# Optimization experiments

Measured on AMD Instinct MI355X. Metric: run time of the kernel, lower is better.

The kernel has to match this reference:

```python
import jax, jax.numpy as jnp
import numpy as np

B, T, D = 2, 2048, 2048
H, KV, HD = 16, 4, 128          # n_heads, n_kv_heads, head_dim
THETA = 10000.0
NREP = H // KV


def _rope_tables(t, hd, dtype):
    inv_freq = 1.0 / (THETA ** (jnp.arange(0, hd, 2, dtype=jnp.float32) / hd))
    pos = jnp.arange(t, dtype=jnp.float32)
    freqs = jnp.outer(pos, inv_freq)            # [T, hd/2]
    emb = jnp.concatenate([freqs, freqs], -1)   # [T, hd]
    return jnp.cos(emb).astype(dtype), jnp.sin(emb).astype(dtype)


def _rotate_half(x):
    a, b = x[..., : x.shape[-1] // 2], x[..., x.shape[-1] // 2 :]
    return jnp.concatenate([-b, a], axis=-1)


def setup_inputs() -> dict:
    key = jax.random.key(0)
    kx, kq, kk, kv, ko = jax.random.split(key, 5)
    s = 1.0 / np.sqrt(D)
    return {
        "x": jax.random.normal(kx, (B, T, D), jnp.float32),
        "Wq": jax.random.normal(kq, (D, H * HD), jnp.float32) * s,
        "Wk": jax.random.normal(kk, (D, KV * HD), jnp.float32) * s,
        "Wv": jax.random.normal(kv, (D, KV * HD), jnp.float32) * s,
        "Wo": jax.random.normal(ko, (H * HD, D), jnp.float32) * s,
    }


def reference(x, Wq, Wk, Wv, Wo):
    b, t, _ = x.shape
    # QKV projections (bias=False)
    q = (x @ Wq).reshape(b, t, H, HD).transpose(0, 2, 1, 3)    # [B,H,T,hd]
    k = (x @ Wk).reshape(b, t, KV, HD).transpose(0, 2, 1, 3)   # [B,KV,T,hd]
    v = (x @ Wv).reshape(b, t, KV, HD).transpose(0, 2, 1, 3)   # [B,KV,T,hd]

    cos, sin = _rope_tables(t, HD, x.dtype)                    # [T,hd]
    q = q * cos + _rotate_half(q) * sin
    k = k * cos + _rotate_half(k) * sin

    # GQA: group query heads onto shared KV heads (no KV replication)
    qg = q.reshape(b, KV, NREP, t, HD)                         # [B,KV,R,T,hd]
    scale = HD ** -0.5
    scores = jnp.einsum("bgrth,bgsh->bgrts", qg, k) * scale    # [B,KV,R,T,T]
    causal = jnp.tril(jnp.ones((t, t), bool))
    scores = jnp.where(causal, scores, jnp.finfo(scores.dtype).min)
    attn = jax.nn.softmax(scores.astype(jnp.float32), axis=-1).astype(x.dtype)
    out = jnp.einsum("bgrts,bgsh->bgrth", attn, v)             # [B,KV,R,T,hd]
    out = out.reshape(b, H, t, HD).transpose(0, 2, 1, 3).reshape(b, t, H * HD)
    return out @ Wo
```

## Files before the change

kernel.cpp:

```cpp
#include <hip/hip_runtime.h>
#include <hip/hip_bf16.h>
#include <type_traits>

#define B_ 2
#define T_ 2048
#define DM_ 2048
#define H_ 16
#define KV_ 4
#define HD_ 128
#define M_ 4096
#define QKVN 3072

typedef __attribute__((ext_vector_type(8))) short bf16x8;
typedef __attribute__((ext_vector_type(4))) float f32x4;
typedef __attribute__((ext_vector_type(4))) short s16x4;
typedef unsigned short u16;
typedef unsigned int u32;
typedef __attribute__((address_space(1))) unsigned int as1_u32;
typedef __attribute__((address_space(3))) unsigned int as3_u32;

__device__ inline u16 f2b(float f){
  __hip_bfloat16 h = __float2bfloat16(f);
  return *reinterpret_cast<u16*>(&h);
}
__device__ inline float b2f(u16 u){
  __hip_bfloat16 h = *reinterpret_cast<__hip_bfloat16*>(&u);
  return __bfloat162float(h);
}
__device__ inline f32x4 mfma16(bf16x8 a, bf16x8 b, f32x4 c){
  return __builtin_amdgcn_mfma_f32_16x16x32_bf16(a, b, c, 0, 0, 0);
}

__global__ void cvt_f32_bf16(const float* __restrict__ in, u16* __restrict__ out){
  int i = (blockIdx.x*256 + threadIdx.x)*4;
  float4 v = *reinterpret_cast<const float4*>(in + i);
  s16x4 o;
  o[0] = (short)f2b(v.x); o[1] = (short)f2b(v.y);
  o[2] = (short)f2b(v.z); o[3] = (short)f2b(v.w);
  *reinterpret_cast<s16x4*>(out + i) = o;
}

__global__ void transpose_cvt(const float* __restrict__ W, u16* __restrict__ Wt, int K, int N){
  __shared__ float tile[32][33];
  const int n0 = blockIdx.x*32, k0 = blockIdx.y*32;
  const int tx = threadIdx.x, ty = threadIdx.y;
#pragma unroll
  for (int i=0;i<4;i++)
    tile[ty+8*i][tx] = W[(size_t)(k0+ty+8*i)*N + n0 + tx];
  __syncthreads();
#pragma unroll
  for (int i=0;i<4;i++)
    Wt[(size_t)(n0+ty+8*i)*K + k0 + tx] = f2b(tile[tx][ty+8*i]);
}

__global__ void transpose_v(const u16* __restrict__ vb, u16* __restrict__ vt){
  __shared__ u16 tile[32][33];
  const int t0 = blockIdx.x*32, d0 = blockIdx.y*32, bk = blockIdx.z;
  const int bb = bk >> 2, kv = bk & 3;
  const int tx = threadIdx.x, ty = threadIdx.y;
#pragma unroll
  for (int i=0;i<4;i++)
    tile[ty+8*i][tx] = vb[(size_t)(bb*T_ + t0+ty+8*i)*QKVN + kv*HD_ + d0 + tx];
  __syncthreads();
#pragma unroll
  for (int i=0;i<4;i++)
    vt[(size_t)(bk*HD_ + d0+ty+8*i)*T_ + t0 + tx] = tile[tx][ty+8*i];
}

__global__ void rope_table(float2* __restrict__ tab){
  int idx = blockIdx.x*256 + threadIdx.x;
  int t = idx >> 6, d = idx & 63;
  float inv = exp2f((float)d * -0.2076205059304601f);
  float sn, cs;
  sincosf((float)t * inv, &sn, &cs);
  tab[idx] = float2{cs, sn};
}

__global__ void rope_apply(u16* __restrict__ qk, const float2* __restrict__ tab,
                           int lognh, int stride){
  int idx = blockIdx.x*256 + threadIdx.x;
  int dp = idx & 31;
  int rh = idx >> 5;
  int nh = 1 << lognh;
  int h = rh & (nh-1);
  int row = rh >> lognh;
  if (row >= M_) return;
  int t = row & (T_-1);
  float4 cn = *reinterpret_cast<const float4*>(tab + t*64 + 2*dp);
  size_t base = (size_t)row*stride + h*HD_ + 2*dp;
  u32 lo = *reinterpret_cast<const u32*>(qk + base);
  u32 hi = *reinterpret_cast<const u32*>(qk + base + 64);
  float a0 = b2f(lo & 0xffff), a1 = b2f(lo >> 16);
  float b0 = b2f(hi & 0xffff), b1 = b2f(hi >> 16);
  u32 nlo = (u32)f2b(a0*cn.x - b0*cn.y) | ((u32)f2b(a1*cn.z - b1*cn.w) << 16);
  u32 nhi = (u32)f2b(b0*cn.x + a0*cn.y) | ((u32)f2b(b1*cn.z + a1*cn.w) << 16);
  *reinterpret_cast<u32*>(qk + base)      = nlo;
  *reinterpret_cast<u32*>(qk + base + 64) = nhi;
}

__device__ inline void cstore(float* p, float v){ *p = v; }
__device__ inline void cstore(u16* p, float v){ *p = f2b(v); }

template<typename CT>
__global__ __launch_bounds__(256) void gemm_bt(const u16* __restrict__ A, const u16* __restrict__ BT,
                                               CT* __restrict__ C, int M, int N, int K)
{
  __shared__ u16 Als[128*64];
  __shared__ u16 Bls[128*64];
  const int tid = threadIdx.x;
  const int wave = tid>>6, lane = tid&63;
  const int gl = lane>>4, qcl = lane&15;
  const int gx = gridDim.x;
  int wid = blockIdx.y*gx + blockIdx.x;
  const int cpx = (gx*gridDim.y) >> 3;
  wid = (wid & 7)*cpx + (wid >> 3);
  const int m0 = (wid / gx)*128, n0 = (wid % gx)*128;
  const int wr = (wave>>1)*64, wc = (wave&1)*64;

  f32x4 acc[4][4];
#pragma unroll
  for (int i=0;i<4;i++)
#pragma unroll
    for (int j=0;j<4;j++) acc[i][j] = f32x4{0.f,0.f,0.f,0.f};

  int rowD[4], colD[4];
#pragma unroll
  for (int p=0;p<4;p++){
    const int D = p*4096 + tid*16;
    rowD[p] = D>>7;
    colD[p] = ((((D>>4)&7) ^ (rowD[p]&7)))*8;
  }

  for (int k0=0; k0<K; k0+=64){
    __syncthreads();
#pragma unroll
    for (int p=0;p<4;p++){
      __builtin_amdgcn_global_load_lds((as1_u32*)(A  + (size_t)(m0+rowD[p])*K + k0 + colD[p]),
                                       (as3_u32*)((char*)Als + p*4096 + wave*1024), 16, 0, 0);
      __builtin_amdgcn_global_load_lds((as1_u32*)(BT + (size_t)(n0+rowD[p])*K + k0 + colD[p]),
                                       (as3_u32*)((char*)Bls + p*4096 + wave*1024), 16, 0, 0);
    }
    __syncthreads();

    bf16x8 af[4][2], bfr[4][2];
#pragma unroll
    for (int mi=0;mi<4;mi++)
#pragma unroll
      for (int kk=0;kk<2;kk++){
        const int row = wr + mi*16 + qcl;
        af[mi][kk] = *reinterpret_cast<const bf16x8*>((char*)Als + row*128 + (((kk<<2)+gl) ^ (qcl&7))*16);
      }
#pragma unroll
    for (int ni=0;ni<4;ni++)
#pragma unroll
      for (int kk=0;kk<2;kk++){
        const int row = wc + ni*16 + qcl;
        bfr[ni][kk] = *reinterpret_cast<const bf16x8*>((char*)Bls + row*128 + (((kk<<2)+gl) ^ (qcl&7))*16);
      }
#pragma unroll
    for (int mi=0;mi<4;mi++)
#pragma unroll
      for (int ni=0;ni<4;ni++)
#pragma unroll
        for (int kk=0;kk<2;kk++)
          acc[mi][ni] = mfma16(af[mi][kk], bfr[ni][kk], acc[mi][ni]);
  }

#pragma unroll
  for (int mi=0;mi<4;mi++)
#pragma unroll
    for (int ni=0;ni<4;ni++)
#pragma unroll
      for (int j=0;j<4;j++){
        int row = m0 + wr + mi*16 + (lane>>4)*4 + j;
        int col = n0 + wc + ni*16 + (lane&15);
        cstore(C + (size_t)row*N + col, acc[mi][ni][j]);
      }
}

__device__ inline const u16* slot_cptr(const u16* pout, const u16* pwt, int u){
  return (u < 4096) ? (pout + (size_t)u*4096) : (pwt + (size_t)(u-4096)*4096);
}

__global__ __launch_bounds__(256, 3) void attn_kernel(const u16* __restrict__ qkv,
                                                      const u16* __restrict__ Vt,
                                                      u16* __restrict__ pout,
                                                      u16* __restrict__ pwt,
                                                      float* __restrict__ ml,
                                                      u16* __restrict__ ao)
{
  __shared__ u16 Ktile[2][4096];
  __shared__ u16 Vtile[2][4096];
  __shared__ u16 plds[4][32*40];
  const int wave = threadIdx.x>>6, lane = threadIdx.x&63;
  const int g = lane>>4, qc = lane&15;

  const int bh = blockIdx.x & 31;
  const int rem = blockIdx.x >> 5;
  int q4, e;
  if (rem < 4)       { q4=0; e=rem; }
  else if (rem < 12) { q4=1; e=rem-4; }
  else if (rem < 24) { q4=2; e=rem-12; }
  else               { q4=3; e=rem-24; }
  const int j  = q4*4 + e/(q4+1);
  const int c  = e%(q4+1);
  const int nc = q4 + 1;
  const int qt = j*4 + wave;
  const int ntg = j*4 + 4;
  const int tstart = 16*c;
  const int tcnt = min(16, ntg - tstart);

  const int h = bh & (H_-1), b = bh >> 4;
  const int kv = h >> 2;

  const u16* qbase = qkv + (size_t)(b*T_ + qt*32)*QKVN + h*HD_ + 8*g;
  bf16x8 qf[2][4];
#pragma unroll
  for (int qs=0; qs<2; qs++)
#pragma unroll
    for (int d4=0; d4<4; d4++)
      qf[qs][d4] = *reinterpret_cast<const bf16x8*>(qbase + (size_t)(qs*16+qc)*QKVN + d4*32);

  const char* Kbase = (const char*)(qkv + (size_t)(b*T_)*QKVN + 2048 + kv*HD_);
  const char* Vbase = (const char*)(Vt + (size_t)(b*KV_+kv)*HD_*T_);
  const char* Ktc = (const char*)&Ktile[0][0];
  const char* Vtc = (const char*)&Vtile[0][0];

  f32x4 oacc[2][8];
#pragma unroll
  for (int qs=0; qs<2; qs++)
#pragma unroll
    for (int dt=0; dt<8; dt++) oacc[qs][dt] = f32x4{0.f,0.f,0.f,0.f};
  float mrun[2] = {-1e30f, -1e30f};
  float lrun[2] = {0.f, 0.f};
  const float SCALE = 0.08838834764831845f;
  const float L2E = 1.4426950408889634f;
  const float DEFER = 8.f;
  u16* pw = &plds[wave][0];

  auto compute = [&](int t, int half, auto mc){
    constexpr bool masked = decltype(mc)::value;
    const int s0 = t*32;
    const int hb = half*8192;
    f32x4 sacc[2][2];
#pragma unroll
    for (int qs=0; qs<2; qs++)
#pragma unroll
      for (int ss=0; ss<2; ss++) sacc[qs][ss] = f32x4{0.f,0.f,0.f,0.f};
    __builtin_amdgcn_s_setprio(1);
#pragma unroll
    for (int d4=0; d4<4; d4++)
#pragma unroll
      for (int ss=0; ss<2; ss++){
        int A = ((ss*16+qc)<<8) + (d4<<6) + (g<<4);
        A ^= (qc&7)<<4;
        bf16x8 kf = *reinterpret_cast<const bf16x8*>(Ktc + hb + A);
#pragma unroll
        for (int qs=0; qs<2; qs++)
          sacc[qs][ss] = mfma16(kf, qf[qs][d4], sacc[qs][ss]);
      }
    __builtin_amdgcn_s_setprio(0);

    float p[2][8], al[2], mnew[2];
#pragma unroll
    for (int qs=0; qs<2; qs++){
      float tm = -1e30f;
#pragma unroll
      for (int ss=0; ss<2; ss++)
#pragma unroll
        for (int jj=0; jj<4; jj++){
          float v = sacc[qs][ss][jj]*SCALE;
          if constexpr (masked){
            int sg = s0 + ss*16 + g*4 + jj;
            if (sg > qt*32 + qs*16 + qc) v = -1e30f;
          }
          p[qs][ss*4+jj] = v;
          tm = fmaxf(tm, v);
        }
      tm = fmaxf(tm, __shfl_xor(tm, 16));
      tm = fmaxf(tm, __shfl_xor(tm, 32));
      mnew[qs] = fmaxf(mrun[qs], tm);
      if (tm - mrun[qs] <= DEFER) mnew[qs] = mrun[qs];
      al[qs] = exp2f((mrun[qs]-mnew[qs])*L2E);
    }
#pragma unroll
    for (int qs=0; qs<2; qs++){
      float rs = 0.f;
#pragma unroll
      for (int i=0;i<8;i++){ p[qs][i] = exp2f((p[qs][i]-mnew[qs])*L2E); rs += p[qs][i]; }
      rs += __shfl_xor(rs, 16);
      rs += __shfl_xor(rs, 32);
      lrun[qs] = lrun[qs]*al[qs] + rs;
      mrun[qs] = mnew[qs];
    }
    if (!__all((al[0]==1.f) & (al[1]==1.f))){
      float aj0[4], aj1[4];
#pragma unroll
      for (int jj=0; jj<4; jj++){
        aj0[jj] = __shfl(al[0], g*4+jj);
        aj1[jj] = __shfl(al[1], g*4+jj);
      }
#pragma unroll
      for (int dt=0; dt<8; dt++)
#pragma unroll
        for (int jj=0; jj<4; jj++){
          oacc[0][dt][jj] *= aj0[jj];
          oacc[1][dt][jj] *= aj1[jj];
        }
    }
#pragma unroll
    for (int qs=0; qs<2; qs++)
#pragma unroll
      for (int ss=0; ss<2; ss++){
        unsigned w0 = (unsigned)f2b(p[qs][ss*4+0]) | ((unsigned)f2b(p[qs][ss*4+1])<<16);
        unsigned w1 = (unsigned)f2b(p[qs][ss*4+2]) | ((unsigned)f2b(p[qs][ss*4+3])<<16);
        *reinterpret_cast<unsigned*>(pw + (qs*16+qc)*40 + ss*16 + g*4)     = w0;
        *reinterpret_cast<unsigned*>(pw + (qs*16+qc)*40 + ss*16 + g*4 + 2) = w1;
      }
    bf16x8 pf[2];
#pragma unroll
    for (int qs=0; qs<2; qs++)
      pf[qs] = *reinterpret_cast<const bf16x8*>(pw + (qs*16+qc)*40 + 8*g);
    __builtin_amdgcn_s_setprio(1);
#pragma unroll
    for (int dt=0; dt<8; dt++){
      int A = ((dt*16+qc)<<6) + (g<<4);
      A ^= ((qc>>1)&3)<<4;
      bf16x8 vf = *reinterpret_cast<const bf16x8*>(Vtc + hb + A);
#pragma unroll
      for (int qs=0; qs<2; qs++)
        oacc[qs][dt] = mfma16(pf[qs], vf, oacc[qs][dt]);
    }
    __builtin_amdgcn_s_setprio(0);
  };
  using Tc = std::integral_constant<bool,true>;
  using Fc = std::integral_constant<bool,false>;

  const int npair = (tcnt+1)>>1;
  for (int ip = 0; ip < npair; ip++){
    const int t0 = tstart + 2*ip;
    const int ntile = min(2, tstart + tcnt - t0);
    __syncthreads();
#pragma unroll
    for (int tt=0; tt<2; tt++){
      if (tt < ntile){
        const size_t r0 = (size_t)(t0+tt)*32;
#pragma unroll
        for (int c2=0; c2<2; c2++){
          const int cc = wave*2 + c2;
          const int D = cc*1024 + lane*16;
          {
            const int LK = D ^ (((D>>8)&7)<<4);
            const char* src = Kbase + (r0 + (size_t)(D>>8))*(QKVN*2) + (LK & 255);
            __builtin_amdgcn_global_load_lds((as1_u32*)src,
              (as3_u32*)((char*)&Ktile[0][0] + tt*8192 + cc*1024), 16, 0, 0);
          }
          {
            const int LV = (D&63) ^ (((D>>7)&3)<<4);
            const char* src = Vbase + ((size_t)(D>>6)*T_ + r0 + (LV>>1))*2;
            __builtin_amdgcn_global_load_lds((as1_u32*)src,
              (as3_u32*)((char*)&Vtile[0][0] + tt*8192 + cc*1024), 16, 0, 0);
          }
        }
      }
    }
    __syncthreads();
    if (t0 < qt)       compute(t0,   0, Fc{});
    else if (t0 == qt) compute(t0,   0, Tc{});
    if (ntile > 1){
      if (t0+1 < qt)       compute(t0+1, 1, Fc{});
      else if (t0+1 == qt) compute(t0+1, 1, Tc{});
    }
  }

  if (nc == 1){
    float lj0[4], lj1[4];
    float li0 = 1.f/lrun[0], li1 = 1.f/lrun[1];
#pragma unroll
    for (int jj=0; jj<4; jj++){
      lj0[jj] = __shfl(li0, g*4+jj);
      lj1[jj] = __shfl(li1, g*4+jj);
    }
    u16* ob = ao + (size_t)(b*T_ + qt*32)*(H_*HD_) + h*HD_;
#pragma unroll
    for (int dt=0; dt<8; dt++)
#pragma unroll
      for (int jj=0; jj<4; jj++){
        ob[(size_t)(g*4+jj)*(H_*HD_) + dt*16 + qc]      = f2b(oacc[0][dt][jj]*lj0[jj]);
        ob[(size_t)(16 + g*4+jj)*(H_*HD_) + dt*16 + qc] = f2b(oacc[1][dt][jj]*lj1[jj]);
      }
  } else {
    int off;
    if (qt < 32)      off = (qt-16)*2;
    else if (qt < 48) off = 32 + (qt-32)*3;
    else              off = 80 + (qt-48)*4;
    const int u = bh*144 + off + c;
    u16* ob = (u < 4096) ? (pout + (size_t)u*4096) : (pwt + (size_t)(u-4096)*4096);
#pragma unroll
    for (int qs=0; qs<2; qs++)
#pragma unroll
      for (int dt=0; dt<8; dt++)
#pragma unroll
        for (int jj=0; jj<4; jj++)
          ob[(size_t)(qs*16 + g*4+jj)*128 + dt*16 + qc] = f2b(oacc[qs][dt][jj]);
    if (lane < 16){
      float* mlb = ml + (size_t)u*64;
#pragma unroll
      for (int qs=0; qs<2; qs++){
        mlb[qs*16 + lane]      = mrun[qs];
        mlb[32 + qs*16 + lane] = lrun[qs];
      }
    }
  }
}

__global__ void combine_kernel(const u16* __restrict__ pout, const u16* __restrict__ pwt,
                               const float* __restrict__ ml, u16* __restrict__ ao)
{
  const float L2E = 1.4426950408889634f;
  int idx = blockIdx.x*256 + threadIdx.x;
  int dg = idx & 15;
  int r  = (idx >> 4) & 31;
  int t  = idx >> 9;
  int bh = t/48, qi = t%48;
  int qt = 16 + qi;
  int nc, off;
  if (qt < 32)      { nc = 2; off = (qt-16)*2; }
  else if (qt < 48) { nc = 3; off = 32 + (qt-32)*3; }
  else              { nc = 4; off = 80 + (qt-48)*4; }
  const int ubase = bh*144 + off;

  float m[4], l[4];
  float M = -1e30f;
#pragma unroll 4
  for (int cc=0; cc<4; cc++){
    if (cc < nc){
      m[cc] = ml[(size_t)(ubase+cc)*64 + r];
      l[cc] = ml[(size_t)(ubase+cc)*64 + 32 + r];
      M = fmaxf(M, m[cc]);
    }
  }
  float acc[8];
#pragma unroll
  for (int i=0;i<8;i++) acc[i] = 0.f;
  float denom = 0.f;
#pragma unroll 4
  for (int cc=0; cc<4; cc++){
    if (cc < nc){
      float w = exp2f((m[cc]-M)*L2E);
      denom += w*l[cc];
      const u16* sp = slot_cptr(pout, pwt, ubase+cc);
      bf16x8 v8 = *reinterpret_cast<const bf16x8*>(sp + (size_t)r*128 + dg*8);
#pragma unroll
      for (int i=0;i<8;i++) acc[i] += w*b2f((u16)v8[i]);
    }
  }
  float inv = 1.f/denom;
  bf16x8 o;
#pragma unroll
  for (int i=0;i<8;i++) o[i] = (short)f2b(acc[i]*inv);
  int b = bh >> 4, h = bh & 15;
  size_t row = (size_t)b*T_ + qt*32 + r;
  *reinterpret_cast<bf16x8*>(ao + row*2048 + h*128 + dg*8) = o;
}

extern "C" void kernel_launch(void* const* d_in, const int* in_sizes, int n_in,
                              void* d_out, int out_size, void* d_ws, size_t ws_size,
                              hipStream_t stream)
{
  const float* x  = (const float*)d_in[0];
  const float* Wq = (const float*)d_in[1];
  const float* Wk = (const float*)d_in[2];
  const float* Wv = (const float*)d_in[3];
  const float* Wo = (const float*)d_in[4];
  float* out = (float*)d_out;

  char* ws = (char*)d_ws;
  size_t off = 0;
  auto carve = [&](size_t bytes)->void*{
    void* p = ws + off; off += (bytes + 255) & ~(size_t)255; return p;
  };
  u16*    xb   = (u16*)carve((size_t)M_*DM_*2);
  u16*    wT   = (u16*)carve((size_t)QKVN*2048*2);
  u16*    woT  = (u16*)carve((size_t)2048*2048*2);
  u16*    qkv  = (u16*)carve((size_t)M_*QKVN*2);
  u16*    vt   = (u16*)carve((size_t)M_*512*2);
  float2* tab  = (float2*)carve((size_t)T_*64*8);
  float*  ml   = (float*)carve((size_t)4608*64*4);
  u16*    ao   = xb;
  u16*    pout = (u16*)d_out;
  u16*    pwt  = wT;

  cvt_f32_bf16<<<8192, 256, 0, stream>>>(x, xb);
  rope_table<<<512, 256, 0, stream>>>(tab);
  transpose_cvt<<<dim3(64,64), dim3(32,8), 0, stream>>>(Wq, wT,               2048, 2048);
  transpose_cvt<<<dim3(16,64), dim3(32,8), 0, stream>>>(Wk, wT + 2048*2048,   2048, 512);
  transpose_cvt<<<dim3(16,64), dim3(32,8), 0, stream>>>(Wv, wT + 2560*2048,   2048, 512);
  transpose_cvt<<<dim3(64,64), dim3(32,8), 0, stream>>>(Wo, woT,              2048, 2048);

  gemm_bt<u16><<<dim3(24,32), 256, 0, stream>>>(xb, wT, qkv, M_, QKVN, 2048);

  rope_apply<<<8192, 256, 0, stream>>>(qkv,        tab, 4, QKVN);
  rope_apply<<<2048, 256, 0, stream>>>(qkv + 2048, tab, 2, QKVN);

  transpose_v<<<dim3(64,4,8), dim3(32,8), 0, stream>>>(qkv + 2560, vt);

  attn_kernel<<<1280, 256, 0, stream>>>(qkv, vt, pout, pwt, ml, ao);
  combine_kernel<<<3072, 256, 0, stream>>>(pout, pwt, ml, ao);

  gemm_bt<float><<<dim3(16,32), 256, 0, stream>>>(ao, woT, out, M_, 2048, 2048);
}
```

Baseline: 243.1 us.

## Double-buffer LDS in projection GEMMs with larger 256-row tiles and 512 threads

Replaces the single-buffered 128x128 GEMM with a templated kernel that prefetches the next K-slice into a second LDS buffer while the current slice is computed. Explicit vmcnt waits and raw barriers replace the two __syncthreads per iteration, and s_setprio raises priority around the MFMA blocks. Tiles grow to 256xBN with 8 waves per block, increasing per-wave reuse. The cost is much more LDS per block (up to 128KB) and far fewer blocks: 192 for the QKV GEMM, which may leave CUs idle.

After: 242.2 us. Within noise of the previous version (-0.4%).

```diff
diff --git a/kernel.cpp b/kernel.cpp
--- a/kernel.cpp
+++ b/kernel.cpp
@@ -101,12 +101,16 @@
 __device__ inline void cstore(float* p, float v){ *p = v; }
 __device__ inline void cstore(u16* p, float v){ *p = f2b(v); }
 
-template<typename CT>
-__global__ __launch_bounds__(256) void gemm_bt(const u16* __restrict__ A, const u16* __restrict__ BT,
-                                               CT* __restrict__ C, int M, int N, int K)
+template<typename CT, int BN, int NWC>
+__global__ __launch_bounds__(512, 2) void gemm_db(const u16* __restrict__ A, const u16* __restrict__ BT,
+                                                  CT* __restrict__ C, int M, int N, int K)
 {
-  __shared__ u16 Als[128*64];
-  __shared__ u16 Bls[128*64];
+  constexpr int AP = 4;
+  constexpr int BP = BN/64;
+  constexpr int MR = 2*NWC;
+  __shared__ u16 Als[2][256*64];
+  __shared__ u16 Bls[2][BN*64];
+
   const int tid = threadIdx.x;
   const int wave = tid>>6, lane = tid&63;
   const int gl = lane>>4, qcl = lane&15;
@@ -114,60 +118,90 @@
   int wid = blockIdx.y*gx + blockIdx.x;
   const int cpx = (gx*gridDim.y) >> 3;
   wid = (wid & 7)*cpx + (wid >> 3);
-  const int m0 = (wid / gx)*128, n0 = (wid % gx)*128;
-  const int wr = (wave>>1)*64, wc = (wave&1)*64;
-
-  f32x4 acc[4][4];
-#pragma unroll
-  for (int i=0;i<4;i++)
+  const int m0 = (wid / gx)*256, n0 = (wid % gx)*BN;
+  const int wr = (wave / NWC)*(16*MR);
+  const int wc = (wave % NWC)*64;
+
+  f32x4 acc[MR][4];
+#pragma unroll
+  for (int i=0;i<MR;i++)
 #pragma unroll
     for (int j=0;j<4;j++) acc[i][j] = f32x4{0.f,0.f,0.f,0.f};
 
-  int rowD[4], colD[4];
-#pragma unroll
-  for (int p=0;p<4;p++){
-    const int D = p*4096 + tid*16;
-    rowD[p] = D>>7;
-    colD[p] = ((((D>>4)&7) ^ (rowD[p]&7)))*8;
-  }
-
-  for (int k0=0; k0<K; k0+=64){
-    __syncthreads();
-#pragma unroll
-    for (int p=0;p<4;p++){
-      __builtin_amdgcn_global_load_lds((as1_u32*)(A  + (size_t)(m0+rowD[p])*K + k0 + colD[p]),
-                                       (as3_u32*)((char*)Als + p*4096 + wave*1024), 16, 0, 0);
-      __builtin_amdgcn_global_load_lds((as1_u32*)(BT + (size_t)(n0+rowD[p])*K + k0 + colD[p]),
-                                       (as3_u32*)((char*)Bls + p*4096 + wave*1024), 16, 0, 0);
-    }
-    __syncthreads();
-
-    bf16x8 af[4][2], bfr[4][2];
-#pragma unroll
-    for (int mi=0;mi<4;mi++)
-#pragma unroll
-      for (int kk=0;kk<2;kk++){
+  const u16* srcA[AP];
+  const u16* srcB[BP];
+#pragma unroll
+  for (int p=0;p<AP;p++){
+    const int D = p*8192 + tid*16;
+    const int row = D>>7;
+    const int colb = (((D>>4)&7) ^ (row&7))*8;
+    srcA[p] = A + (size_t)(m0+row)*K + colb;
+  }
+#pragma unroll
+  for (int p=0;p<BP;p++){
+    const int D = p*8192 + tid*16;
+    const int row = D>>7;
+    const int colb = (((D>>4)&7) ^ (row&7))*8;
+    srcB[p] = BT + (size_t)(n0+row)*K + colb;
+  }
+
+  auto stage = [&](int buf){
+#pragma unroll
+    for (int p=0;p<AP;p++)
+      __builtin_amdgcn_global_load_lds((as1_u32*)srcA[p],
+        (as3_u32*)((char*)&Als[buf][0] + p*8192 + wave*1024), 16, 0, 0);
+#pragma unroll
+    for (int p=0;p<BP;p++)
+      __builtin_amdgcn_global_load_lds((as1_u32*)srcB[p],
+        (as3_u32*)((char*)&Bls[buf][0] + p*8192 + wave*1024), 16, 0, 0);
+#pragma unroll
+    for (int p=0;p<AP;p++) srcA[p] += 64;
+#pragma unroll
+    for (int p=0;p<BP;p++) srcB[p] += 64;
+  };
+
+  auto compute = [&](int buf){
+#pragma unroll
+    for (int kk=0;kk<2;kk++){
+      bf16x8 af[MR], bfr[4];
+#pragma unroll
+      for (int mi=0;mi<MR;mi++){
         const int row = wr + mi*16 + qcl;
-        af[mi][kk] = *reinterpret_cast<const bf16x8*>((char*)Als + row*128 + (((kk<<2)+gl) ^ (qcl&7))*16);
-      }
-#pragma unroll
-    for (int ni=0;ni<4;ni++)
-#pragma unroll
-      for (int kk=0;kk<2;kk++){
+        af[mi] = *reinterpret_cast<const bf16x8*>((char*)&Als[buf][0] + row*128 + (((kk<<2)+gl) ^ (qcl&7))*16);
+      }
+#pragma unroll
+      for (int ni=0;ni<4;ni++){
         const int row = wc + ni*16 + qcl;
-        bfr[ni][kk] = *reinterpret_cast<const bf16x8*>((char*)Bls + row*128 + (((kk<<2)+gl) ^ (qcl&7))*16);
-      }
-#pragma unroll
-    for (int mi=0;mi<4;mi++)
-#pragma unroll
-      for (int ni=0;ni<4;ni++)
-#pragma unroll
-        for (int kk=0;kk<2;kk++)
-          acc[mi][ni] = mfma16(af[mi][kk], bfr[ni][kk], acc[mi][ni]);
-  }
-
-#pragma unroll
-  for (int mi=0;mi<4;mi++)
+        bfr[ni] = *reinterpret_cast<const bf16x8*>((char*)&Bls[buf][0] + row*128 + (((kk<<2)+gl) ^ (qcl&7))*16);
+      }
+      __builtin_amdgcn_s_setprio(1);
+#pragma unroll
+      for (int mi=0;mi<MR;mi++)
+#pragma unroll
+        for (int ni=0;ni<4;ni++)
+          acc[mi][ni] = mfma16(af[mi], bfr[ni], acc[mi][ni]);
+      __builtin_amdgcn_s_setprio(0);
+    }
+  };
+
+  const int NT = K >> 6;
+  stage(0);
+  for (int t=0; t<NT; t++){
+    const int cur = t&1;
+    if (t+1 < NT){
+      stage(cur^1);
+      if constexpr (AP+BP == 8) asm volatile("s_waitcnt vmcnt(8)" ::: "memory");
+      else                      asm volatile("s_waitcnt vmcnt(6)" ::: "memory");
+    } else {
+      asm volatile("s_waitcnt vmcnt(0)" ::: "memory");
+    }
+    __builtin_amdgcn_s_barrier();
+    compute(cur);
+    __builtin_amdgcn_s_barrier();
+  }
+
+#pragma unroll
+  for (int mi=0;mi<MR;mi++)
 #pragma unroll
     for (int ni=0;ni<4;ni++)
 #pragma unroll
@@ -498,7 +532,7 @@
   transpose_cvt<<<dim3(16,64), dim3(32,8), 0, stream>>>(Wv, wT + 2560*2048,   2048, 512);
   transpose_cvt<<<dim3(64,64), dim3(32,8), 0, stream>>>(Wo, woT,              2048, 2048);
 
-  gemm_bt<u16><<<dim3(24,32), 256, 0, stream>>>(xb, wT, qkv, M_, QKVN, 2048);
+  gemm_db<u16,256,4><<<dim3(12,16), 512, 0, stream>>>(xb, wT, qkv, M_, QKVN, 2048);
 
   rope_apply<<<8192, 256, 0, stream>>>(qkv,        tab, 4, QKVN);
   rope_apply<<<2048, 256, 0, stream>>>(qkv + 2048, tab, 2, QKVN);
@@ -508,5 +542,5 @@
   attn_kernel<<<1280, 256, 0, stream>>>(qkv, vt, pout, pwt, ml, ao);
   combine_kernel<<<3072, 256, 0, stream>>>(pout, pwt, ml, ao);
 
-  gemm_bt<float><<<dim3(16,32), 256, 0, stream>>>(ao, woT, out, M_, 2048, 2048);
-}
+  gemm_db<float,128,2><<<dim3(16,16), 512, 0, stream>>>(ao, woT, out, M_, 2048, 2048);
+}
```
